# Optimization experiments

Hardware: AMD Instinct MI355X
Metric: run time of the kernel (lower is better)

Reference implementation:

```python
import jax, jax.numpy as jnp
import numpy as np
from jax import lax

VOCAB = 5000
HIDDEN = 1024
SEQ = 128
BATCH = 64


def setup_inputs() -> dict:
    key = jax.random.key(0)
    ks = jax.random.split(key, 12)
    s = 1.0 / np.sqrt(HIDDEN)
    u = lambda k, shape: jax.random.uniform(k, shape, jnp.float32, -s, s)
    return {
        "x": jax.random.randint(ks[0], (SEQ, BATCH), 0, VOCAB),
        # layer 1: input size = VOCAB
        "W_ih1": u(ks[1], (HIDDEN, VOCAB)),
        "W_hh1": u(ks[2], (HIDDEN, HIDDEN)),
        "b_ih1": u(ks[3], (HIDDEN,)),
        "b_hh1": u(ks[4], (HIDDEN,)),
        # layer 2: input size = HIDDEN
        "W_ih2": u(ks[5], (HIDDEN, HIDDEN)),
        "W_hh2": u(ks[6], (HIDDEN, HIDDEN)),
        "b_ih2": u(ks[7], (HIDDEN,)),
        "b_hh2": u(ks[8], (HIDDEN,)),
        # final projection
        "W_fc": u(ks[9], (VOCAB, HIDDEN)),
        "b_fc": u(ks[10], (VOCAB,)),
    }


def _rnn_layer(x_proj, W_hh, b_hh, h0):
    # x_proj: (S, B, H) precomputed input contribution (incl. b_ih)
    def step(h, xt):
        h = jnp.tanh(xt + h @ W_hh.T + b_hh)
        return h, h
    h_last, ys = lax.scan(step, h0, x_proj)
    return ys, h_last


def reference(x, W_ih1, W_hh1, b_ih1, b_hh1, W_ih2, W_hh2, b_ih2, b_hh2, W_fc, b_fc):
    S, B = x.shape
    H = W_hh1.shape[0]
    h0 = jnp.zeros((B, H), dtype=W_ih1.dtype)
    # one_hot(x) @ W_ih1.T is exactly a row-gather of W_ih1.T
    xp1 = jnp.take(W_ih1.T, x, axis=0) + b_ih1          # (S, B, H)
    y1, h1 = _rnn_layer(xp1, W_hh1, b_hh1, h0)
    xp2 = jnp.einsum("sbh,gh->sbg", y1, W_ih2) + b_ih2  # (S, B, H)
    y2, h2 = _rnn_layer(xp2, W_hh2, b_hh2, h0)
    ans = jnp.einsum("sbh,vh->sbv", y2, W_fc) + b_fc    # (S, B, V)
    state = jnp.stack([h1, h2])                          # (2, B, H)
    return ans, state
```

## Files before the change

kernel.cpp:

```cpp
#include <hip/hip_runtime.h>
#include <hip/hip_bf16.h>

#define VOCAB 5000
#define HIDDEN 1024
#define SEQ 128
#define BATCH 64
#define NBLK 96

typedef __hip_bfloat16 bf16;
typedef short bf16x8 __attribute__((ext_vector_type(8)));
typedef float f32x4 __attribute__((ext_vector_type(4)));

__device__ __forceinline__ float b2f(bf16 v) { return __bfloat162float(v); }

__device__ __forceinline__ bool detect_fp32(const void* w) {
    const unsigned* p = (const unsigned*)w;
    unsigned big = 0;
    #pragma unroll
    for (int i = 0; i < 64; ++i) {
        unsigned e = (p[i] >> 7) & 0xFFu;
        big |= (e >= 127u) ? 1u : 0u;
    }
    return big != 0;
}

__global__ __launch_bounds__(256) void convert_w(const void* __restrict__ src,
                                                 bf16* __restrict__ dst, int n,
                                                 const void* __restrict__ det) {
    const bool f32 = detect_fp32(det);
    int i = (blockIdx.x * 256 + threadIdx.x) * 4;
    if (f32) {
        const float* s = (const float*)src;
        #pragma unroll
        for (int j = 0; j < 4; ++j) if (i + j < n) dst[i + j] = __float2bfloat16(s[i + j]);
    } else {
        const bf16* s = (const bf16*)src;
        #pragma unroll
        for (int j = 0; j < 4; ++j) if (i + j < n) dst[i + j] = s[i + j];
    }
}

__global__ __launch_bounds__(256) void make_bias(const void* __restrict__ a,
                                                 const void* __restrict__ b,
                                                 float* __restrict__ dst, int n,
                                                 const void* __restrict__ det) {
    const bool f32 = detect_fp32(det);
    int i = blockIdx.x * 256 + threadIdx.x;
    if (i >= n) return;
    float v = f32 ? ((const float*)a)[i] : b2f(((const bf16*)a)[i]);
    if (b)  v += f32 ? ((const float*)b)[i] : b2f(((const bf16*)b)[i]);
    dst[i] = v;
}

__device__ __forceinline__ void grid_bar(int* bar, int idx) {
    __syncthreads();
    if (threadIdx.x == 0) {
        __hip_atomic_fetch_add(&bar[idx], 1, __ATOMIC_RELEASE, __HIP_MEMORY_SCOPE_AGENT);
        while (__hip_atomic_load(&bar[idx], __ATOMIC_ACQUIRE, __HIP_MEMORY_SCOPE_AGENT) < NBLK)
            __builtin_amdgcn_s_sleep(2);
    }
    __syncthreads();
}

__global__ __launch_bounds__(256, 1) void rnn_persistent(
    const int*  __restrict__ x,
    const void* __restrict__ Wih1raw,
    const bf16* __restrict__ whh1,
    const bf16* __restrict__ wih2,
    const bf16* __restrict__ whh2,
    const float* __restrict__ bias1,
    const float* __restrict__ bias2,
    bf16* __restrict__ y1r,
    bf16* __restrict__ y2,
    int* __restrict__ bar)
{
    extern __shared__ bf16 lds[];
    const int bid  = blockIdx.x;
    const int tid  = threadIdx.x;
    const int wave = tid >> 6;
    const int lane = tid & 63;
    const int q    = lane >> 4;
    const int l15  = lane & 15;
    const size_t BH = (size_t)BATCH * HIDDEN;

    const bool l1  = (bid < 32);
    const int  n0  = l1 ? bid * 32 : (bid - 32) * 16;
    const int  cpr = l1 ? 128 : 256;
    const int  rows = l1 ? 32 : 16;

    for (int idx = tid; idx < rows * cpr; idx += 256) {
        const int r = idx / 128; const int rr = l1 ? r : (r >> 1);
        const int c = idx - (idx / cpr) * cpr;
        const int row = idx / cpr;
        const bf16* src;
        if (l1) src = whh1 + (size_t)(n0 + row) * HIDDEN + c * 8;
        else {
            const bf16* W = (c < 128) ? wih2 : whh2;
            src = W + (size_t)(n0 + row) * HIDDEN + (c & 127) * 8;
        }
        (void)r; (void)rr;
        *(bf16x8*)&lds[(size_t)(row * cpr + (c ^ (row & 7))) * 8] = *(const bf16x8*)src;
    }
    __syncthreads();

    const bool f32in = detect_fp32(Wih1raw);
    const int  mrow  = wave * 16 + l15;

    float breg[2];
    if (l1) { breg[0] = bias1[n0 + l15]; breg[1] = bias1[n0 + 16 + l15]; }
    else    { breg[0] = bias2[n0 + l15]; breg[1] = 0.f; }

    for (int s = 0; s <= SEQ; ++s) {
        if (l1) {
            if (s < SEQ) {
                const int step = s;
                float xg[2][4];
                #pragma unroll
                for (int r = 0; r < 4; ++r) {
                    const int b  = wave * 16 + q * 4 + r;
                    const int xv = x[step * BATCH + b];
                    #pragma unroll
                    for (int t = 0; t < 2; ++t) {
                        const size_t gi = (size_t)(n0 + t * 16 + l15) * VOCAB + xv;
                        xg[t][r] = f32in ? ((const float*)Wih1raw)[gi]
                                         : b2f(((const bf16*)Wih1raw)[gi]);
                    }
                }
                f32x4 acc0 = {0.f,0.f,0.f,0.f}, acc1 = {0.f,0.f,0.f,0.f};
                if (step > 0) {
                    const bf16* arow = y1r + (size_t)((step - 1) & 1) * BH
                                           + (size_t)mrow * HIDDEN + q * 8;
                    for (int k0 = 0; k0 < HIDDEN; k0 += 32) {
                        bf16x8 af = *(const bf16x8*)(arow + k0);
                        const int chb = ((k0 >> 3) + q);
                        bf16x8 b0 = *(const bf16x8*)&lds[(size_t)((l15     ) * 128 + (chb ^ (l15 & 7))) * 8];
                        bf16x8 b1 = *(const bf16x8*)&lds[(size_t)((l15 + 16) * 128 + (chb ^ (l15 & 7))) * 8];
                        acc0 = __builtin_amdgcn_mfma_f32_16x16x32_bf16(af, b0, acc0, 0, 0, 0);
                        acc1 = __builtin_amdgcn_mfma_f32_16x16x32_bf16(af, b1, acc1, 0, 0, 0);
                    }
                }
                bf16* out = y1r + (size_t)(step & 1) * BH;
                #pragma unroll
                for (int t = 0; t < 2; ++t) {
                    const int i = n0 + t * 16 + l15;
                    const f32x4 a = t ? acc1 : acc0;
                    #pragma unroll
                    for (int r = 0; r < 4; ++r) {
                        const int b = wave * 16 + q * 4 + r;
                        float v = a[r] + breg[t] + xg[t][r];
                        out[(size_t)b * HIDDEN + i] = __float2bfloat16(tanhf(v));
                    }
                }
            }
        } else {
            if (s >= 1) {
                const int st = s - 1;
                f32x4 acc0 = {0.f,0.f,0.f,0.f}, acc1 = {0.f,0.f,0.f,0.f};
                const bf16* a1row = y1r + (size_t)(st & 1) * BH
                                        + (size_t)mrow * HIDDEN + q * 8;
                for (int k0 = 0; k0 < 1024; k0 += 64) {
                    bf16x8 afa = *(const bf16x8*)(a1row + k0);
                    bf16x8 afb = *(const bf16x8*)(a1row + k0 + 32);
                    const int ca = (((k0      ) >> 3) + q) ^ (l15 & 7);
                    const int cb = (((k0 + 32 ) >> 3) + q) ^ (l15 & 7);
                    bf16x8 ba = *(const bf16x8*)&lds[(size_t)(l15 * 256 + ca) * 8];
                    bf16x8 bb = *(const bf16x8*)&lds[(size_t)(l15 * 256 + cb) * 8];
                    acc0 = __builtin_amdgcn_mfma_f32_16x16x32_bf16(afa, ba, acc0, 0, 0, 0);
                    acc1 = __builtin_amdgcn_mfma_f32_16x16x32_bf16(afb, bb, acc1, 0, 0, 0);
                }
                if (st > 0) {
                    const bf16* a2row = y2 + (size_t)(st - 1) * BH
                                           + (size_t)mrow * HIDDEN + q * 8;
                    for (int k0 = 0; k0 < 1024; k0 += 64) {
                        bf16x8 afa = *(const bf16x8*)(a2row + k0);
                        bf16x8 afb = *(const bf16x8*)(a2row + k0 + 32);
                        const int ca = (((k0 + 1024) >> 3) + q) ^ (l15 & 7);
                        const int cb = (((k0 + 1056) >> 3) + q) ^ (l15 & 7);
                        bf16x8 ba = *(const bf16x8*)&lds[(size_t)(l15 * 256 + ca) * 8];
                        bf16x8 bb = *(const bf16x8*)&lds[(size_t)(l15 * 256 + cb) * 8];
                        acc0 = __builtin_amdgcn_mfma_f32_16x16x32_bf16(afa, ba, acc0, 0, 0, 0);
                        acc1 = __builtin_amdgcn_mfma_f32_16x16x32_bf16(afb, bb, acc1, 0, 0, 0);
                    }
                }
                bf16* out = y2 + (size_t)st * BH;
                const int i = n0 + l15;
                #pragma unroll
                for (int r = 0; r < 4; ++r) {
                    const int b = wave * 16 + q * 4 + r;
                    float v = acc0[r] + acc1[r] + breg[0];
                    out[(size_t)b * HIDDEN + i] = __float2bfloat16(tanhf(v));
                }
            }
        }
        grid_bar(bar, s);
    }
}

__global__ __launch_bounds__(256) void proj(
    const bf16* __restrict__ y2, const bf16* __restrict__ Wfc,
    const float* __restrict__ bfc, void* __restrict__ outp,
    const void* __restrict__ det)
{
    const int bn = blockIdx.x;
    const int bm = blockIdx.y;
    const int wave = threadIdx.x >> 6;
    const int lane = threadIdx.x & 63;
    const int q = lane >> 4, l15 = lane & 15;
    const int wm = wave & 1, wn = wave >> 1;
    const int m0 = bm * 64 + wm * 32;
    const int n0 = bn * 128 + wn * 64;

    f32x4 acc[2][4];
    #pragma unroll
    for (int i = 0; i < 2; ++i)
        #pragma unroll
        for (int t = 0; t < 4; ++t) acc[i][t] = (f32x4){0.f, 0.f, 0.f, 0.f};

    const bf16x8 zf = (bf16x8){0,0,0,0,0,0,0,0};
    const bf16* a0p = y2 + (size_t)(m0 + l15) * HIDDEN + q * 8;
    const bf16* a1p = a0p + (size_t)16 * HIDDEN;

    for (int k0 = 0; k0 < HIDDEN; k0 += 32) {
        bf16x8 af0 = *(const bf16x8*)(a0p + k0);
        bf16x8 af1 = *(const bf16x8*)(a1p + k0);
        #pragma unroll
        for (int t = 0; t < 4; ++t) {
            const int n = n0 + t * 16 + l15;
            bf16x8 bfr = (n < VOCAB)
                ? *(const bf16x8*)(Wfc + (size_t)n * HIDDEN + k0 + q * 8) : zf;
            acc[0][t] = __builtin_amdgcn_mfma_f32_16x16x32_bf16(af0, bfr, acc[0][t], 0, 0, 0);
            acc[1][t] = __builtin_amdgcn_mfma_f32_16x16x32_bf16(af1, bfr, acc[1][t], 0, 0, 0);
        }
    }

    const bool f32out = detect_fp32(det);

    #pragma unroll
    for (int t = 0; t < 4; ++t) {
        const int col = n0 + t * 16 + l15;
        if (col >= VOCAB) continue;
        const float bias = bfc[col];
        #pragma unroll
        for (int i = 0; i < 2; ++i)
            #pragma unroll
            for (int r = 0; r < 4; ++r) {
                const int row = m0 + i * 16 + q * 4 + r;
                const float v = acc[i][t][r] + bias;
                const size_t o = (size_t)row * VOCAB + col;
                if (f32out) ((float*)outp)[o] = v;
                else        ((bf16*)outp)[o] = __float2bfloat16(v);
            }
    }
}

__global__ __launch_bounds__(256) void state_copy(
    const bf16* __restrict__ y1r, const bf16* __restrict__ y2,
    void* __restrict__ outp, const void* __restrict__ det)
{
    const bool f32out = detect_fp32(det);
    const int t = blockIdx.x * blockDim.x + threadIdx.x;
    const int BH = BATCH * HIDDEN;
    const size_t ofs = (size_t)SEQ * BATCH * VOCAB;
    float v;
    if (t < BH) v = b2f(y1r[(size_t)((SEQ - 1) & 1) * BH + t]);
    else        v = b2f(y2[(size_t)(SEQ - 1) * BH + (t - BH)]);
    if (f32out) ((float*)outp)[ofs + t] = v;
    else        ((bf16*)outp)[ofs + t] = __float2bfloat16(v);
}

extern "C" void kernel_launch(void* const* d_in, const int* in_sizes, int n_in,
                              void* d_out, int out_size, void* d_ws, size_t ws_size,
                              hipStream_t stream) {
    const int*  x       = (const int*)d_in[0];
    const void* Wih1raw = d_in[1];
    const void* Whh1raw = d_in[2];
    const void* bih1    = d_in[3];
    const void* bhh1    = d_in[4];
    const void* Wih2raw = d_in[5];
    const void* Whh2raw = d_in[6];
    const void* bih2    = d_in[7];
    const void* bhh2    = d_in[8];
    const void* Wfcraw  = d_in[9];
    const void* bfcraw  = d_in[10];

    char* wsb = (char*)d_ws;
    int*   bar   = (int*)wsb;
    bf16*  y2    = (bf16*)(wsb + 1024);
    bf16*  y1r   = y2   + (size_t)SEQ * BATCH * HIDDEN;
    bf16*  whh1  = y1r  + (size_t)2 * BATCH * HIDDEN;
    bf16*  wih2  = whh1 + (size_t)HIDDEN * HIDDEN;
    bf16*  whh2  = wih2 + (size_t)HIDDEN * HIDDEN;
    bf16*  wfcb  = whh2 + (size_t)HIDDEN * HIDDEN;
    float* bias1 = (float*)(wfcb + (size_t)VOCAB * HIDDEN);
    float* bias2 = bias1 + HIDDEN;
    float* bfcf  = bias2 + HIDDEN;

    hipMemsetAsync(bar, 0, (SEQ + 1) * sizeof(int), stream);

    const int HH = HIDDEN * HIDDEN, VH = VOCAB * HIDDEN;
    convert_w<<<(HH + 1023) / 1024, 256, 0, stream>>>(Whh1raw, whh1, HH, Wih1raw);
    convert_w<<<(HH + 1023) / 1024, 256, 0, stream>>>(Wih2raw, wih2, HH, Wih1raw);
    convert_w<<<(HH + 1023) / 1024, 256, 0, stream>>>(Whh2raw, whh2, HH, Wih1raw);
    convert_w<<<(VH + 1023) / 1024, 256, 0, stream>>>(Wfcraw,  wfcb, VH, Wih1raw);
    make_bias<<<(HIDDEN + 255) / 256, 256, 0, stream>>>(bih1, bhh1, bias1, HIDDEN, Wih1raw);
    make_bias<<<(HIDDEN + 255) / 256, 256, 0, stream>>>(bih2, bhh2, bias2, HIDDEN, Wih1raw);
    make_bias<<<(VOCAB + 255) / 256, 256, 0, stream>>>(bfcraw, nullptr, bfcf, VOCAB, Wih1raw);

    rnn_persistent<<<NBLK, 256, 65536, stream>>>(x, Wih1raw, whh1, wih2, whh2,
                                                 bias1, bias2, y1r, y2, bar);

    proj<<<dim3(40, 128), 256, 0, stream>>>(y2, wfcb, bfcf, d_out, Wih1raw);
    state_copy<<<(2 * BATCH * HIDDEN) / 256, 256, 0, stream>>>(y1r, y2, d_out, Wih1raw);
}
```

Before: 2.342 ms.

## Replace grid barrier with per-step flags and pipeline RNN layers via ring buffer

```diff
diff --git a/kernel.cpp b/kernel.cpp
--- a/kernel.cpp
+++ b/kernel.cpp
@@ -5,7 +5,10 @@
 #define HIDDEN 1024
 #define SEQ 128
 #define BATCH 64
-#define NBLK 96
+#define L1NB 16
+#define L2NB 32
+#define NBLK (L1NB + L2NB)
+#define RING 8
 
 typedef __hip_bfloat16 bf16;
 typedef short bf16x8 __attribute__((ext_vector_type(8)));
@@ -52,14 +55,16 @@
     dst[i] = v;
 }
 
-__device__ __forceinline__ void grid_bar(int* bar, int idx) {
-    __syncthreads();
-    if (threadIdx.x == 0) {
-        __hip_atomic_fetch_add(&bar[idx], 1, __ATOMIC_RELEASE, __HIP_MEMORY_SCOPE_AGENT);
-        while (__hip_atomic_load(&bar[idx], __ATOMIC_ACQUIRE, __HIP_MEMORY_SCOPE_AGENT) < NBLK)
-            __builtin_amdgcn_s_sleep(2);
-    }
-    __syncthreads();
+__device__ __forceinline__ void wait_flag(int* flag, int target) {
+    int v = __hip_atomic_load(flag, __ATOMIC_RELAXED, __HIP_MEMORY_SCOPE_AGENT);
+    int n = 0;
+    while (v < target) {
+        __builtin_amdgcn_s_sleep(1);
+        if ((++n & 63) == 0)
+            v = __hip_atomic_load(flag, __ATOMIC_ACQUIRE, __HIP_MEMORY_SCOPE_AGENT);
+        else
+            v = __hip_atomic_load(flag, __ATOMIC_RELAXED, __HIP_MEMORY_SCOPE_AGENT);
+    }
 }
 
 __global__ __launch_bounds__(256, 1) void rnn_persistent(
@@ -72,7 +77,8 @@
     const float* __restrict__ bias2,
     bf16* __restrict__ y1r,
     bf16* __restrict__ y2,
-    int* __restrict__ bar)
+    int* __restrict__ f1,
+    int* __restrict__ f2)
 {
     extern __shared__ bf16 lds[];
     const int bid  = blockIdx.x;
@@ -82,117 +88,145 @@
     const int q    = lane >> 4;
     const int l15  = lane & 15;
     const size_t BH = (size_t)BATCH * HIDDEN;
-
-    const bool l1  = (bid < 32);
-    const int  n0  = l1 ? bid * 32 : (bid - 32) * 16;
-    const int  cpr = l1 ? 128 : 256;
-    const int  rows = l1 ? 32 : 16;
-
-    for (int idx = tid; idx < rows * cpr; idx += 256) {
-        const int r = idx / 128; const int rr = l1 ? r : (r >> 1);
-        const int c = idx - (idx / cpr) * cpr;
-        const int row = idx / cpr;
-        const bf16* src;
-        if (l1) src = whh1 + (size_t)(n0 + row) * HIDDEN + c * 8;
-        else {
-            const bf16* W = (c < 128) ? wih2 : whh2;
-            src = W + (size_t)(n0 + row) * HIDDEN + (c & 127) * 8;
-        }
-        (void)r; (void)rr;
-        *(bf16x8*)&lds[(size_t)(row * cpr + (c ^ (row & 7))) * 8] = *(const bf16x8*)src;
-    }
-    __syncthreads();
-
     const bool f32in = detect_fp32(Wih1raw);
     const int  mrow  = wave * 16 + l15;
 
-    float breg[2];
-    if (l1) { breg[0] = bias1[n0 + l15]; breg[1] = bias1[n0 + 16 + l15]; }
-    else    { breg[0] = bias2[n0 + l15]; breg[1] = 0.f; }
-
-    for (int s = 0; s <= SEQ; ++s) {
-        if (l1) {
-            if (s < SEQ) {
-                const int step = s;
-                float xg[2][4];
-                #pragma unroll
-                for (int r = 0; r < 4; ++r) {
-                    const int b  = wave * 16 + q * 4 + r;
-                    const int xv = x[step * BATCH + b];
+    if (bid < L1NB) {
+        const int n0 = bid * 64;
+        for (int idx = tid; idx < 64 * 128; idx += 256) {
+            const int row = idx >> 7, c = idx & 127;
+            *(bf16x8*)&lds[(size_t)((row << 7) + (c ^ (row & 7))) * 8] =
+                *(const bf16x8*)(whh1 + (size_t)(n0 + row) * HIDDEN + c * 8);
+        }
+        __syncthreads();
+
+        float breg[4];
+        #pragma unroll
+        for (int t = 0; t < 4; ++t) breg[t] = bias1[n0 + t * 16 + l15];
+
+        for (int s = 0; s < SEQ; ++s) {
+            float xg[4][4];
+            {
+                int xv[4];
+                #pragma unroll
+                for (int r = 0; r < 4; ++r) xv[r] = x[s * BATCH + wave * 16 + q * 4 + r];
+                #pragma unroll
+                for (int t = 0; t < 4; ++t)
                     #pragma unroll
-                    for (int t = 0; t < 2; ++t) {
-                        const size_t gi = (size_t)(n0 + t * 16 + l15) * VOCAB + xv;
+                    for (int r = 0; r < 4; ++r) {
+                        const size_t gi = (size_t)(n0 + t * 16 + l15) * VOCAB + xv[r];
                         xg[t][r] = f32in ? ((const float*)Wih1raw)[gi]
                                          : b2f(((const bf16*)Wih1raw)[gi]);
                     }
-                }
-                f32x4 acc0 = {0.f,0.f,0.f,0.f}, acc1 = {0.f,0.f,0.f,0.f};
-                if (step > 0) {
-                    const bf16* arow = y1r + (size_t)((step - 1) & 1) * BH
-                                           + (size_t)mrow * HIDDEN + q * 8;
-                    for (int k0 = 0; k0 < HIDDEN; k0 += 32) {
-                        bf16x8 af = *(const bf16x8*)(arow + k0);
-                        const int chb = ((k0 >> 3) + q);
-                        bf16x8 b0 = *(const bf16x8*)&lds[(size_t)((l15     ) * 128 + (chb ^ (l15 & 7))) * 8];
-                        bf16x8 b1 = *(const bf16x8*)&lds[(size_t)((l15 + 16) * 128 + (chb ^ (l15 & 7))) * 8];
-                        acc0 = __builtin_amdgcn_mfma_f32_16x16x32_bf16(af, b0, acc0, 0, 0, 0);
-                        acc1 = __builtin_amdgcn_mfma_f32_16x16x32_bf16(af, b1, acc1, 0, 0, 0);
+            }
+            if (tid == 0) {
+                if (s >= 1)    wait_flag(&f1[s - 1], L1NB);
+                if (s >= RING) wait_flag(&f2[s - RING], L2NB);
+                __builtin_amdgcn_fence(__ATOMIC_ACQUIRE, "agent");
+            }
+            __syncthreads();
+
+            f32x4 acc[4];
+            #pragma unroll
+            for (int t = 0; t < 4; ++t) acc[t] = (f32x4){0.f,0.f,0.f,0.f};
+            if (s > 0) {
+                const bf16* arow = y1r + (size_t)((s - 1) & (RING - 1)) * BH
+                                       + (size_t)mrow * HIDDEN + q * 8;
+                for (int k0 = 0; k0 < HIDDEN; k0 += 32) {
+                    bf16x8 af = *(const bf16x8*)(arow + k0);
+                    const int chb = (k0 >> 3) + q;
+                    #pragma unroll
+                    for (int t = 0; t < 4; ++t) {
+                        const int row = t * 16 + l15;
+                        bf16x8 bw = *(const bf16x8*)&lds[(size_t)((row << 7) + (chb ^ (row & 7))) * 8];
+                        acc[t] = __builtin_amdgcn_mfma_f32_16x16x32_bf16(af, bw, acc[t], 0, 0, 0);
                     }
                 }
-                bf16* out = y1r + (size_t)(step & 1) * BH;
-                #pragma unroll
-                for (int t = 0; t < 2; ++t) {
-                    const int i = n0 + t * 16 + l15;
-                    const f32x4 a = t ? acc1 : acc0;
-                    #pragma unroll
-                    for (int r = 0; r < 4; ++r) {
-                        const int b = wave * 16 + q * 4 + r;
-                        float v = a[r] + breg[t] + xg[t][r];
-                        out[(size_t)b * HIDDEN + i] = __float2bfloat16(tanhf(v));
-                    }
-                }
-            }
-        } else {
-            if (s >= 1) {
-                const int st = s - 1;
-                f32x4 acc0 = {0.f,0.f,0.f,0.f}, acc1 = {0.f,0.f,0.f,0.f};
-                const bf16* a1row = y1r + (size_t)(st & 1) * BH
-                                        + (size_t)mrow * HIDDEN + q * 8;
-                for (int k0 = 0; k0 < 1024; k0 += 64) {
-                    bf16x8 afa = *(const bf16x8*)(a1row + k0);
-                    bf16x8 afb = *(const bf16x8*)(a1row + k0 + 32);
-                    const int ca = (((k0      ) >> 3) + q) ^ (l15 & 7);
-                    const int cb = (((k0 + 32 ) >> 3) + q) ^ (l15 & 7);
-                    bf16x8 ba = *(const bf16x8*)&lds[(size_t)(l15 * 256 + ca) * 8];
-                    bf16x8 bb = *(const bf16x8*)&lds[(size_t)(l15 * 256 + cb) * 8];
-                    acc0 = __builtin_amdgcn_mfma_f32_16x16x32_bf16(afa, ba, acc0, 0, 0, 0);
-                    acc1 = __builtin_amdgcn_mfma_f32_16x16x32_bf16(afb, bb, acc1, 0, 0, 0);
-                }
-                if (st > 0) {
-                    const bf16* a2row = y2 + (size_t)(st - 1) * BH
-                                           + (size_t)mrow * HIDDEN + q * 8;
-                    for (int k0 = 0; k0 < 1024; k0 += 64) {
-                        bf16x8 afa = *(const bf16x8*)(a2row + k0);
-                        bf16x8 afb = *(const bf16x8*)(a2row + k0 + 32);
-                        const int ca = (((k0 + 1024) >> 3) + q) ^ (l15 & 7);
-                        const int cb = (((k0 + 1056) >> 3) + q) ^ (l15 & 7);
-                        bf16x8 ba = *(const bf16x8*)&lds[(size_t)(l15 * 256 + ca) * 8];
-                        bf16x8 bb = *(const bf16x8*)&lds[(size_t)(l15 * 256 + cb) * 8];
-                        acc0 = __builtin_amdgcn_mfma_f32_16x16x32_bf16(afa, ba, acc0, 0, 0, 0);
-                        acc1 = __builtin_amdgcn_mfma_f32_16x16x32_bf16(afb, bb, acc1, 0, 0, 0);
-                    }
-                }
-                bf16* out = y2 + (size_t)st * BH;
-                const int i = n0 + l15;
+            }
+            bf16* out = y1r + (size_t)(s & (RING - 1)) * BH;
+            #pragma unroll
+            for (int t = 0; t < 4; ++t) {
+                const int i = n0 + t * 16 + l15;
                 #pragma unroll
                 for (int r = 0; r < 4; ++r) {
                     const int b = wave * 16 + q * 4 + r;
-                    float v = acc0[r] + acc1[r] + breg[0];
-                    out[(size_t)b * HIDDEN + i] = __float2bfloat16(tanhf(v));
-                }
-            }
-        }
-        grid_bar(bar, s);
+                    out[(size_t)b * HIDDEN + i] =
+                        __float2bfloat16(tanhf(acc[t][r] + breg[t] + xg[t][r]));
+                }
+            }
+            __syncthreads();
+            if (tid == 0)
+                __hip_atomic_fetch_add(&f1[s], 1, __ATOMIC_RELEASE, __HIP_MEMORY_SCOPE_AGENT);
+        }
+    } else {
+        const int n0 = (bid - L1NB) * 32;
+        for (int idx = tid; idx < 32 * 256; idx += 256) {
+            const int row = idx >> 8, c = idx & 255;
+            const bf16* W = (c < 128) ? wih2 : whh2;
+            *(bf16x8*)&lds[(size_t)((row << 8) + (c ^ (row & 7))) * 8] =
+                *(const bf16x8*)(W + (size_t)(n0 + row) * HIDDEN + (c & 127) * 8);
+        }
+        __syncthreads();
+
+        float breg[2];
+        #pragma unroll
+        for (int t = 0; t < 2; ++t) breg[t] = bias2[n0 + t * 16 + l15];
+
+        for (int st = 0; st < SEQ; ++st) {
+            if (tid == 0) {
+                wait_flag(&f1[st], L1NB);
+                if (st >= 1) wait_flag(&f2[st - 1], L2NB);
+                __builtin_amdgcn_fence(__ATOMIC_ACQUIRE, "agent");
+            }
+            __syncthreads();
+
+            f32x4 acc[2];
+            #pragma unroll
+            for (int t = 0; t < 2; ++t) acc[t] = (f32x4){0.f,0.f,0.f,0.f};
+
+            {
+                const bf16* arow = y1r + (size_t)(st & (RING - 1)) * BH
+                                       + (size_t)mrow * HIDDEN + q * 8;
+                for (int k0 = 0; k0 < HIDDEN; k0 += 32) {
+                    bf16x8 af = *(const bf16x8*)(arow + k0);
+                    const int chb = (k0 >> 3) + q;
+                    #pragma unroll
+                    for (int t = 0; t < 2; ++t) {
+                        const int row = t * 16 + l15;
+                        bf16x8 bw = *(const bf16x8*)&lds[(size_t)((row << 8) + (chb ^ (row & 7))) * 8];
+                        acc[t] = __builtin_amdgcn_mfma_f32_16x16x32_bf16(af, bw, acc[t], 0, 0, 0);
+                    }
+                }
+            }
+            if (st > 0) {
+                const bf16* arow = y2 + (size_t)(st - 1) * BH
+                                      + (size_t)mrow * HIDDEN + q * 8;
+                for (int k0 = 0; k0 < HIDDEN; k0 += 32) {
+                    bf16x8 af = *(const bf16x8*)(arow + k0);
+                    const int chb = 128 + (k0 >> 3) + q;
+                    #pragma unroll
+                    for (int t = 0; t < 2; ++t) {
+                        const int row = t * 16 + l15;
+                        bf16x8 bw = *(const bf16x8*)&lds[(size_t)((row << 8) + (chb ^ (row & 7))) * 8];
+                        acc[t] = __builtin_amdgcn_mfma_f32_16x16x32_bf16(af, bw, acc[t], 0, 0, 0);
+                    }
+                }
+            }
+            bf16* out = y2 + (size_t)st * BH;
+            #pragma unroll
+            for (int t = 0; t < 2; ++t) {
+                const int i = n0 + t * 16 + l15;
+                #pragma unroll
+                for (int r = 0; r < 4; ++r) {
+                    const int b = wave * 16 + q * 4 + r;
+                    out[(size_t)b * HIDDEN + i] =
+                        __float2bfloat16(tanhf(acc[t][r] + breg[t]));
+                }
+            }
+            __syncthreads();
+            if (tid == 0)
+                __hip_atomic_fetch_add(&f2[st], 1, __ATOMIC_RELEASE, __HIP_MEMORY_SCOPE_AGENT);
+        }
     }
 }
 
@@ -201,20 +235,21 @@
     const float* __restrict__ bfc, void* __restrict__ outp,
     const void* __restrict__ det)
 {
-    const int bn = blockIdx.x;
-    const int bm = blockIdx.y;
+    __shared__ bf16 cbuf[64 * 256];
+    const int bm = blockIdx.x;
+    const int bn = blockIdx.y;
     const int wave = threadIdx.x >> 6;
     const int lane = threadIdx.x & 63;
     const int q = lane >> 4, l15 = lane & 15;
     const int wm = wave & 1, wn = wave >> 1;
     const int m0 = bm * 64 + wm * 32;
-    const int n0 = bn * 128 + wn * 64;
-
-    f32x4 acc[2][4];
+    const int n0 = bn * 256 + wn * 128;
+
+    f32x4 acc[2][8];
     #pragma unroll
     for (int i = 0; i < 2; ++i)
         #pragma unroll
-        for (int t = 0; t < 4; ++t) acc[i][t] = (f32x4){0.f, 0.f, 0.f, 0.f};
+        for (int t = 0; t < 8; ++t) acc[i][t] = (f32x4){0.f,0.f,0.f,0.f};
 
     const bf16x8 zf = (bf16x8){0,0,0,0,0,0,0,0};
     const bf16* a0p = y2 + (size_t)(m0 + l15) * HIDDEN + q * 8;
@@ -224,32 +259,56 @@
         bf16x8 af0 = *(const bf16x8*)(a0p + k0);
         bf16x8 af1 = *(const bf16x8*)(a1p + k0);
         #pragma unroll
-        for (int t = 0; t < 4; ++t) {
+        for (int t = 0; t < 8; ++t) {
             const int n = n0 + t * 16 + l15;
-            bf16x8 bfr = (n < VOCAB)
+            bf16x8 bw = (n < VOCAB)
                 ? *(const bf16x8*)(Wfc + (size_t)n * HIDDEN + k0 + q * 8) : zf;
-            acc[0][t] = __builtin_amdgcn_mfma_f32_16x16x32_bf16(af0, bfr, acc[0][t], 0, 0, 0);
-            acc[1][t] = __builtin_amdgcn_mfma_f32_16x16x32_bf16(af1, bfr, acc[1][t], 0, 0, 0);
+            acc[0][t] = __builtin_amdgcn_mfma_f32_16x16x32_bf16(af0, bw, acc[0][t], 0, 0, 0);
+            acc[1][t] = __builtin_amdgcn_mfma_f32_16x16x32_bf16(af1, bw, acc[1][t], 0, 0, 0);
         }
     }
 
     const bool f32out = detect_fp32(det);
 
+    if (f32out) {
+        #pragma unroll
+        for (int t = 0; t < 8; ++t) {
+            const int col = n0 + t * 16 + l15;
+            if (col >= VOCAB) continue;
+            const float bias = bfc[col];
+            #pragma unroll
+            for (int i = 0; i < 2; ++i)
+                #pragma unroll
+                for (int r = 0; r < 4; ++r) {
+                    const int row = m0 + i * 16 + q * 4 + r;
+                    ((float*)outp)[(size_t)row * VOCAB + col] = acc[i][t][r] + bias;
+                }
+        }
+        return;
+    }
+
     #pragma unroll
-    for (int t = 0; t < 4; ++t) {
-        const int col = n0 + t * 16 + l15;
-        if (col >= VOCAB) continue;
-        const float bias = bfc[col];
+    for (int t = 0; t < 8; ++t) {
+        const int col  = n0 + t * 16 + l15;
+        const int cloc = wn * 128 + t * 16 + l15;
+        const float bias = (col < VOCAB) ? bfc[col] : 0.f;
         #pragma unroll
         for (int i = 0; i < 2; ++i)
             #pragma unroll
             for (int r = 0; r < 4; ++r) {
-                const int row = m0 + i * 16 + q * 4 + r;
-                const float v = acc[i][t][r] + bias;
-                const size_t o = (size_t)row * VOCAB + col;
-                if (f32out) ((float*)outp)[o] = v;
-                else        ((bf16*)outp)[o] = __float2bfloat16(v);
-            }
+                const int rloc = wm * 32 + i * 16 + q * 4 + r;
+                cbuf[rloc * 256 + cloc] = __float2bfloat16(acc[i][t][r] + bias);
+            }
+    }
+    __syncthreads();
+    bf16* ob = (bf16*)outp;
+    for (int cidx = threadIdx.x; cidx < 64 * 32; cidx += 256) {
+        const int row = cidx >> 5;
+        const int c8  = (cidx & 31) * 8;
+        const int gcol = bn * 256 + c8;
+        if (gcol < VOCAB)
+            *(bf16x8*)(ob + (size_t)(bm * 64 + row) * VOCAB + gcol) =
+                *(const bf16x8*)&cbuf[row * 256 + c8];
     }
 }
 
@@ -262,7 +321,7 @@
     const int BH = BATCH * HIDDEN;
     const size_t ofs = (size_t)SEQ * BATCH * VOCAB;
     float v;
-    if (t < BH) v = b2f(y1r[(size_t)((SEQ - 1) & 1) * BH + t]);
+    if (t < BH) v = b2f(y1r[(size_t)((SEQ - 1) & (RING - 1)) * BH + t]);
     else        v = b2f(y2[(size_t)(SEQ - 1) * BH + (t - BH)]);
     if (f32out) ((float*)outp)[ofs + t] = v;
     else        ((bf16*)outp)[ofs + t] = __float2bfloat16(v);
@@ -284,10 +343,11 @@
     const void* bfcraw  = d_in[10];
 
     char* wsb = (char*)d_ws;
-    int*   bar   = (int*)wsb;
+    int*   f1    = (int*)wsb;
+    int*   f2    = f1 + SEQ;
     bf16*  y2    = (bf16*)(wsb + 1024);
     bf16*  y1r   = y2   + (size_t)SEQ * BATCH * HIDDEN;
-    bf16*  whh1  = y1r  + (size_t)2 * BATCH * HIDDEN;
+    bf16*  whh1  = y1r  + (size_t)RING * BATCH * HIDDEN;
     bf16*  wih2  = whh1 + (size_t)HIDDEN * HIDDEN;
     bf16*  whh2  = wih2 + (size_t)HIDDEN * HIDDEN;
     bf16*  wfcb  = whh2 + (size_t)HIDDEN * HIDDEN;
@@ -295,7 +355,7 @@
     float* bias2 = bias1 + HIDDEN;
     float* bfcf  = bias2 + HIDDEN;
 
-    hipMemsetAsync(bar, 0, (SEQ + 1) * sizeof(int), stream);
+    hipMemsetAsync(f1, 0, 2 * SEQ * sizeof(int), stream);
 
     const int HH = HIDDEN * HIDDEN, VH = VOCAB * HIDDEN;
     convert_w<<<(HH + 1023) / 1024, 256, 0, stream>>>(Whh1raw, whh1, HH, Wih1raw);
@@ -306,9 +366,9 @@
     make_bias<<<(HIDDEN + 255) / 256, 256, 0, stream>>>(bih2, bhh2, bias2, HIDDEN, Wih1raw);
     make_bias<<<(VOCAB + 255) / 256, 256, 0, stream>>>(bfcraw, nullptr, bfcf, VOCAB, Wih1raw);
 
-    rnn_persistent<<<NBLK, 256, 65536, stream>>>(x, Wih1raw, whh1, wih2, whh2,
-                                                 bias1, bias2, y1r, y2, bar);
-
-    proj<<<dim3(40, 128), 256, 0, stream>>>(y2, wfcb, bfcf, d_out, Wih1raw);
+    rnn_persistent<<<NBLK, 256, 131072, stream>>>(x, Wih1raw, whh1, wih2, whh2,
+                                                  bias1, bias2, y1r, y2, f1, f2);
+
+    proj<<<dim3(128, 20), 256, 0, stream>>>(y2, wfcb, bfcf, d_out, Wih1raw);
     state_copy<<<(2 * BATCH * HIDDEN) / 256, 256, 0, stream>>>(y1r, y2, d_out, Wih1raw);
 }
```

Result: no change. 2.335 ms (-0.3%).
